# Optimization experiments

Measured on AMD Instinct MI355X. Metric: run time of the kernel, lower is better.

Reference implementation:

```python
import jax, jax.numpy as jnp
import numpy as np

B, NPG, C = 16, 4096, 256          # graphs, nodes per graph per type, feat dim
N = B * NPG                        # nodes per type
E = N * 16                         # edges per edge type (avg degree 16)
RATIO = 0.25
K = int(np.ceil(RATIO * NPG))      # top-k nodes per graph per type


def setup_inputs() -> dict:
    key = jax.random.key(0)
    ks = jax.random.split(key, 16)
    s = 1.0 / np.sqrt(C)
    inp = {
        "x_inst": jax.random.normal(ks[0], (N, C), jnp.float32),
        "x_data": jax.random.normal(ks[1], (N, C), jnp.float32),
        "w_kqv_inst": jax.random.normal(ks[2], (C, 3), jnp.float32) * s,
        "b_kqv_inst": jnp.zeros((3,), jnp.float32),
        "w_kqv_data": jax.random.normal(ks[3], (C, 3), jnp.float32) * s,
        "b_kqv_data": jnp.zeros((3,), jnp.float32),
        "w_out_inst": jax.random.normal(ks[4], (1, 1), jnp.float32),
        "b_out_inst": jnp.zeros((1,), jnp.float32),
        "w_out_data": jax.random.normal(ks[5], (1, 1), jnp.float32),
        "b_out_data": jnp.zeros((1,), jnp.float32),
        "krel_w": jax.random.normal(ks[6], (3,), jnp.float32),
        "krel_b": jnp.zeros((3,), jnp.float32),
        "vrel_w": jax.random.normal(ks[7], (3,), jnp.float32),
        "vrel_b": jnp.zeros((3,), jnp.float32),
        "p_rel": jnp.ones((3,), jnp.float32),
        "ei_i2d": jax.random.randint(ks[8], (2, E), 0, N, jnp.int32),
        "ei_d2i": jax.random.randint(ks[9], (2, E), 0, N, jnp.int32),
        "ei_i2i": jax.random.randint(ks[10], (2, E), 0, N, jnp.int32),
        "batch_inst": jnp.repeat(jnp.arange(B, dtype=jnp.int32), NPG),
        "batch_data": jnp.repeat(jnp.arange(B, dtype=jnp.int32), NPG),
    }
    return inp


def _hgt_scores(x_inst, x_data, w_kqv_inst, b_kqv_inst, w_kqv_data, b_kqv_data,
                w_out_inst, b_out_inst, w_out_data, b_out_data,
                krel_w, krel_b, vrel_w, vrel_b, p_rel,
                ei_i2d, ei_d2i, ei_i2i):
    # HGTConv with out_channels=1, heads=1 -> H=1, D=1 (k,q,v scalar per node)
    kqv_i = x_inst @ w_kqv_inst + b_kqv_inst   # [N,3]
    kqv_d = x_data @ w_kqv_data + b_kqv_data
    k_i, q_i, v_i = kqv_i[:, 0], kqv_i[:, 1], kqv_i[:, 2]
    k_d, q_d, v_d = kqv_d[:, 0], kqv_d[:, 1], kqv_d[:, 2]
    # dst offsets follow node-type order: inst=0, data=N
    q_glob = jnp.concatenate([q_i, q_d])       # [2N]
    Ntot = 2 * N

    def edge_terms(k_src, v_src, ei, t, dst_off):
        s, d = ei[0], ei[1]
        ke = k_src[s] * krel_w[t] + krel_b[t]  # per-relation 1x1 k_rel
        ve = v_src[s] * vrel_w[t] + vrel_b[t]  # per-relation 1x1 v_rel
        dg = d + dst_off
        logit = q_glob[dg] * ke * p_rel[t]     # (q_i*k_j).sum * p_rel / sqrt(D=1)
        return logit, ve, dg

    l0, v0, d0 = edge_terms(k_i, v_i, ei_i2d, 0, N)  # inst->data (dst=data)
    l1, v1, d1 = edge_terms(k_d, v_d, ei_d2i, 1, 0)  # data->inst (dst=inst)
    l2, v2, d2 = edge_terms(k_i, v_i, ei_i2i, 2, 0)  # inst->inst (dst=inst)
    logits = jnp.concatenate([l0, l1, l2])
    vals = jnp.concatenate([v0, v1, v2])
    dst = jnp.concatenate([d0, d1, d2])

    # segment softmax over incoming edges of each destination node
    m = jax.ops.segment_max(logits, dst, num_segments=Ntot)
    m = jnp.where(jnp.isfinite(m), m, 0.0)
    ex = jnp.exp(logits - m[dst])
    den = jax.ops.segment_sum(ex, dst, num_segments=Ntot)
    alpha = ex / den[dst]
    a = jax.ops.segment_sum(alpha * vals, dst, num_segments=Ntot)  # [2N]

    # out_lin (1->1) per node type; skip inactive (1 != 256); GELU (exact)
    s_i = jax.nn.gelu(a[:N, None] * w_out_inst[0, 0] + b_out_inst, approximate=False)
    s_d = jax.nn.gelu(a[N:, None] * w_out_data[0, 0] + b_out_data, approximate=False)
    return s_i, s_d  # [N,1] each


def _pool(x, score):
    # per-graph top-k on score, gate by tanh(score), mean over selected
    sv = score[:, 0].reshape(B, NPG)
    xv = x.reshape(B, NPG, -1)
    topv, topi = jax.lax.top_k(sv, K)                      # [B,K]
    xs = jnp.take_along_axis(xv, topi[:, :, None], axis=1)  # [B,K,C]
    return (xs * jnp.tanh(topv)[:, :, None]).mean(axis=1)   # [B,C]


def reference(x_inst, x_data, w_kqv_inst, b_kqv_inst, w_kqv_data, b_kqv_data,
              w_out_inst, b_out_inst, w_out_data, b_out_data,
              krel_w, krel_b, vrel_w, vrel_b, p_rel,
              ei_i2d, ei_d2i, ei_i2i, batch_inst, batch_data):
    # batch_* are uniform [B x NPG] blocks; pooling uses reshape equivalently.
    s_i, s_d = _hgt_scores(x_inst, x_data, w_kqv_inst, b_kqv_inst,
                           w_kqv_data, b_kqv_data, w_out_inst, b_out_inst,
                           w_out_data, b_out_data, krel_w, krel_b,
                           vrel_w, vrel_b, p_rel, ei_i2d, ei_d2i, ei_i2i)
    return jnp.concatenate([_pool(x_inst, s_i), _pool(x_data, s_d)], axis=-1)  # [B, 2C]
```

## Files before the change

### kernel.cpp

```cpp
#include <hip/hip_runtime.h>
#include <math.h>

constexpr int BB   = 16;
constexpr int NPGc = 4096;
constexpr int Cc   = 256;
constexpr int Nc   = BB * NPGc;
constexpr int Ec   = Nc * 16;
constexpr int Kc   = 1024;
constexpr int NBUK = 512;
constexpr int BUKW = 256;
constexpr int CHUNK = 8192;
constexpr int NCHUNK = (3 * Ec) / CHUNK;

__device__ __forceinline__ unsigned fkey(float f) {
    int b = __float_as_int(f);
    unsigned u = (unsigned)b;
    return (b < 0) ? ~u : (u | 0x80000000u);
}
__device__ __forceinline__ float inv_fkey(unsigned u) {
    unsigned b = (u & 0x80000000u) ? (u ^ 0x80000000u) : ~u;
    return __int_as_float((int)b);
}

__global__ __launch_bounds__(256) void kqv_kernel(
    const float* __restrict__ x_inst, const float* __restrict__ x_data,
    const float* __restrict__ w_inst, const float* __restrict__ b_inst,
    const float* __restrict__ w_data, const float* __restrict__ b_data,
    float2* __restrict__ kv_i, float2* __restrict__ kv_d,
    float* __restrict__ q_glob)
{
    int tid  = threadIdx.x;
    int wave = tid >> 6, lane = tid & 63;
    int grp  = lane >> 4, l = lane & 15;
    int g    = blockIdx.x * 16 + wave * 4 + grp;
    int row0 = g * 2;
    int side = (row0 >= Nc) ? 1 : 0;
    int node0 = row0 - side * Nc;
    const float* x  = side ? x_data : x_inst;
    const float* w  = side ? w_data : w_inst;
    const float* bp = side ? b_data : b_inst;
    float2* kv = side ? kv_d : kv_i;

    float wr[48];
#pragma unroll
    for (int it = 0; it < 4; ++it) {
        const float4* wv = (const float4*)(w + (it * 64 + l * 4) * 3);
        float4 f0 = wv[0], f1 = wv[1], f2 = wv[2];
        wr[it*12+0]=f0.x; wr[it*12+1]=f0.y; wr[it*12+2]=f0.z; wr[it*12+3]=f0.w;
        wr[it*12+4]=f1.x; wr[it*12+5]=f1.y; wr[it*12+6]=f1.z; wr[it*12+7]=f1.w;
        wr[it*12+8]=f2.x; wr[it*12+9]=f2.y; wr[it*12+10]=f2.z; wr[it*12+11]=f2.w;
    }
    float b0 = bp[0], b1 = bp[1], b2 = bp[2];

    const float4* rp = (const float4*)(x + (size_t)node0 * Cc);
    float4 xv[2][4];
#pragma unroll
    for (int r = 0; r < 2; ++r)
#pragma unroll
        for (int it = 0; it < 4; ++it)
            xv[r][it] = rp[r * 64 + it * 16 + l];

#pragma unroll
    for (int r = 0; r < 2; ++r) {
        float kk = 0.f, qq = 0.f, vv = 0.f;
#pragma unroll
        for (int it = 0; it < 4; ++it) {
            float xs[4] = {xv[r][it].x, xv[r][it].y, xv[r][it].z, xv[r][it].w};
#pragma unroll
            for (int u = 0; u < 4; ++u) {
                float xd = xs[u];
                kk = fmaf(xd, wr[it * 12 + u * 3 + 0], kk);
                qq = fmaf(xd, wr[it * 12 + u * 3 + 1], qq);
                vv = fmaf(xd, wr[it * 12 + u * 3 + 2], vv);
            }
        }
#pragma unroll
        for (int off = 8; off; off >>= 1) {
            kk += __shfl_xor(kk, off, 64);
            qq += __shfl_xor(qq, off, 64);
            vv += __shfl_xor(vv, off, 64);
        }
        if (l == 0) {
            int node = node0 + r;
            kv[node] = make_float2(kk + b0, vv + b2);
            q_glob[side * Nc + node] = qq + b1;
        }
    }
}

__global__ __launch_bounds__(256) void count_kernel(
    const int* __restrict__ ei0, const int* __restrict__ ei1,
    const int* __restrict__ ei2, unsigned* __restrict__ bucket_cnt)
{
    __shared__ unsigned hist[NBUK];
    int tid = threadIdx.x;
    for (int j = tid; j < NBUK; j += 256) hist[j] = 0;
    __syncthreads();
    unsigned base = blockIdx.x * (unsigned)CHUNK;
    int t = (int)(base >> 20);
    unsigned i0 = base & (unsigned)(Ec - 1);
    const int* ei = (t == 0) ? ei0 : (t == 1) ? ei1 : ei2;
    int off = (t == 0) ? Nc : 0;
    const int4* dv = (const int4*)(ei + Ec + i0);
#pragma unroll 4
    for (int j = 0; j < CHUNK / 1024; ++j) {
        int4 d4 = dv[j * 256 + tid];
        atomicAdd(&hist[(unsigned)(d4.x + off) >> 8], 1u);
        atomicAdd(&hist[(unsigned)(d4.y + off) >> 8], 1u);
        atomicAdd(&hist[(unsigned)(d4.z + off) >> 8], 1u);
        atomicAdd(&hist[(unsigned)(d4.w + off) >> 8], 1u);
    }
    __syncthreads();
    for (int j = tid; j < NBUK; j += 256)
        if (hist[j]) atomicAdd(&bucket_cnt[j], hist[j]);
}

__global__ __launch_bounds__(NBUK) void scan_kernel(
    const unsigned* __restrict__ bucket_cnt,
    unsigned* __restrict__ bucket_base, unsigned* __restrict__ bucket_fill)
{
    __shared__ unsigned s[NBUK];
    int t = threadIdx.x;
    unsigned mine = bucket_cnt[t];
    s[t] = mine;
    __syncthreads();
    for (int off = 1; off < NBUK; off <<= 1) {
        unsigned v = (t >= off) ? s[t - off] : 0u;
        __syncthreads();
        s[t] += v;
        __syncthreads();
    }
    unsigned ex = s[t] - mine;
    bucket_base[t] = ex;
    bucket_fill[t] = ex;
    if (t == NBUK - 1) bucket_base[NBUK] = s[t];
}

__global__ __launch_bounds__(256) void fill_kernel(
    const int* __restrict__ ei0, const int* __restrict__ ei1,
    const int* __restrict__ ei2, unsigned* __restrict__ bucket_fill,
    unsigned* __restrict__ sorted)
{
    __shared__ unsigned hist[NBUK];
    __shared__ unsigned res[NBUK];
    int tid = threadIdx.x;
    for (int j = tid; j < NBUK; j += 256) hist[j] = 0;
    __syncthreads();
    unsigned base = blockIdx.x * (unsigned)CHUNK;
    int t = (int)(base >> 20);
    unsigned i0 = base & (unsigned)(Ec - 1);
    const int* ei = (t == 0) ? ei0 : (t == 1) ? ei1 : ei2;
    int off = (t == 0) ? Nc : 0;
    const int4* dv = (const int4*)(ei + Ec + i0);
    const int4* sv = (const int4*)(ei + i0);
#pragma unroll 4
    for (int j = 0; j < CHUNK / 1024; ++j) {
        int4 d4 = dv[j * 256 + tid];
        atomicAdd(&hist[(unsigned)(d4.x + off) >> 8], 1u);
        atomicAdd(&hist[(unsigned)(d4.y + off) >> 8], 1u);
        atomicAdd(&hist[(unsigned)(d4.z + off) >> 8], 1u);
        atomicAdd(&hist[(unsigned)(d4.w + off) >> 8], 1u);
    }
    __syncthreads();
    for (int j = tid; j < NBUK; j += 256) {
        unsigned h = hist[j];
        res[j] = h ? atomicAdd(&bucket_fill[j], h) : 0u;
    }
    __syncthreads();
#pragma unroll 4
    for (int j = 0; j < CHUNK / 1024; ++j) {
        int4 d4 = dv[j * 256 + tid];
        int4 s4 = sv[j * 256 + tid];
        int dd[4] = {d4.x, d4.y, d4.z, d4.w};
        int ss[4] = {s4.x, s4.y, s4.z, s4.w};
#pragma unroll
        for (int u = 0; u < 4; ++u) {
            int dg  = dd[u] + off;
            int bkt = dg >> 8;
            unsigned pos = atomicAdd(&res[bkt], 1u);
            sorted[pos] =
                (unsigned)ss[u] | ((unsigned)t << 16) | ((unsigned)(dg & 255) << 18);
        }
    }
}

__global__ __launch_bounds__(512) void bucket_accum_kernel(
    const unsigned* __restrict__ bucket_base, const unsigned* __restrict__ sorted,
    const float* __restrict__ krel_w, const float* __restrict__ krel_b,
    const float* __restrict__ vrel_w, const float* __restrict__ vrel_b,
    const float* __restrict__ p_rel,
    const float2* __restrict__ kv_i, const float2* __restrict__ kv_d,
    const float* __restrict__ q_glob,
    float* __restrict__ den, float* __restrict__ num)
{
    __shared__ float den_l[2 * BUKW];
    __shared__ float num_l[2 * BUKW];
    __shared__ float q_l[BUKW];
    int tid = threadIdx.x;
    int b   = blockIdx.x;
    den_l[tid] = 0.0f; num_l[tid] = 0.0f;
    if (tid < BUKW) q_l[tid] = q_glob[b * BUKW + tid];
    float kw0 = krel_w[0], kw1 = krel_w[1], kw2 = krel_w[2];
    float kb0 = krel_b[0], kb1 = krel_b[1], kb2 = krel_b[2];
    float vw0 = vrel_w[0], vw1 = vrel_w[1], vw2 = vrel_w[2];
    float vb0 = vrel_b[0], vb1 = vrel_b[1], vb2 = vrel_b[2];
    float pr0 = p_rel[0],  pr1 = p_rel[1],  pr2 = p_rel[2];
    unsigned beg = bucket_base[b], end = bucket_base[b + 1];
    int rep = tid & 1;
    __syncthreads();

    for (unsigned e = beg + tid; e < end; e += 512) {
        unsigned r = sorted[e];
        int s    = (int)(r & 0xFFFFu);
        int t    = (int)((r >> 16) & 3u);
        int low8 = (int)((r >> 18) & 255u);
        float2 kvv = (t == 1) ? kv_d[s] : kv_i[s];
        float kwt = (t == 0) ? kw0 : (t == 1) ? kw1 : kw2;
        float kbt = (t == 0) ? kb0 : (t == 1) ? kb1 : kb2;
        float vwt = (t == 0) ? vw0 : (t == 1) ? vw1 : vw2;
        float vbt = (t == 0) ? vb0 : (t == 1) ? vb1 : vb2;
        float prt = (t == 0) ? pr0 : (t == 1) ? pr1 : pr2;
        float ke = fmaf(kvv.x, kwt, kbt);
        float ve = fmaf(kvv.y, vwt, vbt);
        float logit = q_l[low8] * ke * prt;
        float ex = __expf(fminf(logit, 80.0f));
        int slot = low8 * 2 + rep;
        __hip_atomic_fetch_add(&den_l[slot], ex, __ATOMIC_RELAXED,
                               __HIP_MEMORY_SCOPE_WORKGROUP);
        __hip_atomic_fetch_add(&num_l[slot], ex * ve, __ATOMIC_RELAXED,
                               __HIP_MEMORY_SCOPE_WORKGROUP);
    }
    __syncthreads();
    if (tid < BUKW) {
        den[b * BUKW + tid] = den_l[tid * 2] + den_l[tid * 2 + 1];
        num[b * BUKW + tid] = num_l[tid * 2] + num_l[tid * 2 + 1];
    }
}

__global__ __launch_bounds__(1024) void select_kernel(
    const float* __restrict__ den, const float* __restrict__ num,
    const float* __restrict__ w_out_inst, const float* __restrict__ b_out_inst,
    const float* __restrict__ w_out_data, const float* __restrict__ b_out_data,
    int* __restrict__ sel_idx, float* __restrict__ sel_w)
{
    __shared__ unsigned keys[NPGc];
    __shared__ unsigned hist[2048];
    __shared__ unsigned wsum[16];
    __shared__ unsigned short cand[NPGc];
    __shared__ unsigned sh_bin1, sh_rem1, sh_bin2, sh_rem2, sh_cnt, sh_nc;

    int tid  = threadIdx.x;
    int seg  = blockIdx.x;
    int side = seg >> 4;
    int b    = seg & 15;
    float wo = side ? w_out_data[0] : w_out_inst[0];
    float bo = side ? b_out_data[0] : b_out_inst[0];
    int base_node = side * Nc + b * NPGc;
    int base_sel  = seg * Kc;

    unsigned myk[4]; int myj[4];
#pragma unroll
    for (int p = 0; p < 4; ++p) {
        int j = p * 1024 + tid;
        float dn = den[base_node + j];
        float a  = (dn > 0.0f) ? num[base_node + j] / dn : 0.0f;
        float z  = fmaf(a, wo, bo);
        float s  = 0.5f * z * (1.0f + erff(z * 0.70710678f));
        unsigned k32 = fkey(s);
        keys[j] = k32; myk[p] = k32; myj[p] = j;
    }
    if (tid == 0) { sh_cnt = 0; sh_nc = 0; }
    hist[tid] = 0; hist[tid + 1024] = 0;
    __syncthreads();

#pragma unroll
    for (int p = 0; p < 4; ++p) atomicAdd(&hist[myk[p] >> 21], 1u);
    __syncthreads();
    {
        unsigned g0 = hist[2047 - 2 * tid];
        unsigned g1 = hist[2046 - 2 * tid];
        unsigned x = g0 + g1;
        int lane = tid & 63;
#pragma unroll
        for (int off = 1; off < 64; off <<= 1) {
            unsigned y = __shfl_up(x, off, 64);
            if (lane >= off) x += y;
        }
        if (lane == 63) wsum[tid >> 6] = x;
        __syncthreads();
        if (tid < 16) {
            unsigned v = wsum[tid];
#pragma unroll
            for (int off = 1; off < 16; off <<= 1) {
                unsigned y = __shfl_up(v, off, 64);
                if (tid >= off) v += y;
            }
            wsum[tid] = v;
        }
        __syncthreads();
        unsigned basew = (tid >= 64) ? wsum[(tid >> 6) - 1] : 0u;
        unsigned incl  = basew + x;
        unsigned incl0 = incl - g1;
        unsigned K = Kc;
        if (incl0 >= K && incl0 - g0 < K) { sh_bin1 = 2047 - 2 * tid; sh_rem1 = K - (incl0 - g0); }
        if (incl  >= K && incl0     < K) { sh_bin1 = 2046 - 2 * tid; sh_rem1 = K - incl0; }
    }
    __syncthreads();
    unsigned bin1 = sh_bin1, rem1 = sh_rem1;
    hist[tid] = 0; hist[tid + 1024] = 0;
    __syncthreads();

#pragma unroll
    for (int p = 0; p < 4; ++p)
        if ((myk[p] >> 21) == bin1)
            atomicAdd(&hist[(myk[p] >> 10) & 2047u], 1u);
    __syncthreads();
    {
        unsigned g0 = hist[2047 - 2 * tid];
        unsigned g1 = hist[2046 - 2 * tid];
        unsigned x = g0 + g1;
        int lane = tid & 63;
#pragma unroll
        for (int off = 1; off < 64; off <<= 1) {
            unsigned y = __shfl_up(x, off, 64);
            if (lane >= off) x += y;
        }
        if (lane == 63) wsum[tid >> 6] = x;
        __syncthreads();
        if (tid < 16) {
            unsigned v = wsum[tid];
#pragma unroll
            for (int off = 1; off < 16; off <<= 1) {
                unsigned y = __shfl_up(v, off, 64);
                if (tid >= off) v += y;
            }
            wsum[tid] = v;
        }
        __syncthreads();
        unsigned basew = (tid >= 64) ? wsum[(tid >> 6) - 1] : 0u;
        unsigned incl  = basew + x;
        unsigned incl0 = incl - g1;
        unsigned K = rem1;
        if (incl0 >= K && incl0 - g0 < K) { sh_bin2 = 2047 - 2 * tid; sh_rem2 = K - (incl0 - g0); }
        if (incl  >= K && incl0     < K) { sh_bin2 = 2046 - 2 * tid; sh_rem2 = K - incl0; }
    }
    __syncthreads();
    unsigned pref22 = (bin1 << 11) | sh_bin2;
    unsigned rem2 = sh_rem2;

#pragma unroll
    for (int p = 0; p < 4; ++p) {
        unsigned top22 = myk[p] >> 10;
        if (top22 > pref22) {
            unsigned pos = atomicAdd(&sh_cnt, 1u);
            sel_idx[base_sel + pos] = myj[p];
            sel_w[base_sel + pos]   = tanhf(inv_fkey(myk[p]));
        } else if (top22 == pref22) {
            unsigned cp = atomicAdd(&sh_nc, 1u);
            cand[cp] = (unsigned short)myj[p];
        }
    }
    __syncthreads();

    unsigned nc = sh_nc;
    for (unsigned c = tid; c < nc; c += 1024) {
        int j = cand[c];
        unsigned k32 = keys[j];
        unsigned rank = 0;
        for (unsigned q = 0; q < nc; ++q) {
            int jq = cand[q];
            unsigned kq = keys[jq];
            rank += (kq > k32 || (kq == k32 && jq < j)) ? 1u : 0u;
        }
        if (rank < rem2) {
            unsigned pos = atomicAdd(&sh_cnt, 1u);
            sel_idx[base_sel + pos] = j;
            sel_w[base_sel + pos]   = tanhf(inv_fkey(k32));
        }
    }
}

__global__ __launch_bounds__(1024) void pool_kernel(
    const float* __restrict__ x_inst, const float* __restrict__ x_data,
    const int* __restrict__ sel_idx, const float* __restrict__ sel_w,
    float* __restrict__ out)
{
    __shared__ int   ridx[64];
    __shared__ float rw[64];
    __shared__ float accs[256];
    int tid   = threadIdx.x;
    int blk   = blockIdx.x;
    int seg   = blk >> 4;
    int chunk = blk & 15;
    int side  = seg >> 4;
    int b     = seg & 15;
    if (tid < 64) {
        ridx[tid] = sel_idx[seg * Kc + chunk * 64 + tid];
        rw[tid]   = sel_w[seg * Kc + chunk * 64 + tid];
    }
    if (tid < 256) accs[tid] = 0.0f;
    __syncthreads();
    const float* x = side ? x_data : x_inst;
    int w = tid >> 6, l = tid & 63;
    float ax = 0.f, ay = 0.f, az = 0.f, aw = 0.f;
#pragma unroll
    for (int r = 0; r < 4; ++r) {
        int   row = ridx[w * 4 + r];
        float wt  = rw[w * 4 + r];
        float4 xv = ((const float4*)(x + ((size_t)(b * NPGc + row)) * Cc))[l];
        ax = fmaf(xv.x, wt, ax); ay = fmaf(xv.y, wt, ay);
        az = fmaf(xv.z, wt, az); aw = fmaf(xv.w, wt, aw);
    }
    atomicAdd(&accs[l * 4 + 0], ax);
    atomicAdd(&accs[l * 4 + 1], ay);
    atomicAdd(&accs[l * 4 + 2], az);
    atomicAdd(&accs[l * 4 + 3], aw);
    __syncthreads();
    if (tid < 256)
        unsafeAtomicAdd(&out[b * 512 + side * 256 + tid], accs[tid] * (1.0f / (float)Kc));
}

extern "C" void kernel_launch(void* const* d_in, const int* in_sizes, int n_in,
                              void* d_out, int out_size, void* d_ws, size_t ws_size,
                              hipStream_t stream) {
    const float* x_inst     = (const float*)d_in[0];
    const float* x_data     = (const float*)d_in[1];
    const float* w_kqv_inst = (const float*)d_in[2];
    const float* b_kqv_inst = (const float*)d_in[3];
    const float* w_kqv_data = (const float*)d_in[4];
    const float* b_kqv_data = (const float*)d_in[5];
    const float* w_out_inst = (const float*)d_in[6];
    const float* b_out_inst = (const float*)d_in[7];
    const float* w_out_data = (const float*)d_in[8];
    const float* b_out_data = (const float*)d_in[9];
    const float* krel_w     = (const float*)d_in[10];
    const float* krel_b     = (const float*)d_in[11];
    const float* vrel_w     = (const float*)d_in[12];
    const float* vrel_b     = (const float*)d_in[13];
    const float* p_rel      = (const float*)d_in[14];
    const int*   ei_i2d     = (const int*)d_in[15];
    const int*   ei_d2i     = (const int*)d_in[16];
    const int*   ei_i2i     = (const int*)d_in[17];
    float* out = (float*)d_out;

    char* ws = (char*)d_ws;
    float2* kv_i   = (float2*)ws;
    float2* kv_d   = kv_i + Nc;
    float*  q_glob = (float*)(kv_d + Nc);
    float*  den    = q_glob + 2 * Nc;
    float*  num    = den + 2 * Nc;
    unsigned* bucket_cnt  = (unsigned*)(num + 2 * Nc);
    unsigned* bucket_base = bucket_cnt + NBUK;
    unsigned* bucket_fill = bucket_base + NBUK + 1;
    int*      sel_idx     = (int*)(bucket_fill + NBUK);
    float*    sel_w       = (float*)(sel_idx + 32 * Kc);
    unsigned* sorted      = (unsigned*)(sel_w + 32 * Kc);

    hipMemsetAsync(bucket_cnt, 0, NBUK * sizeof(unsigned), stream);
    hipMemsetAsync(d_out, 0, (size_t)out_size * sizeof(float), stream);

    count_kernel<<<NCHUNK, 256, 0, stream>>>(ei_i2d, ei_d2i, ei_i2i, bucket_cnt);
    scan_kernel<<<1, NBUK, 0, stream>>>(bucket_cnt, bucket_base, bucket_fill);
    fill_kernel<<<NCHUNK, 256, 0, stream>>>(ei_i2d, ei_d2i, ei_i2i,
                                            bucket_fill, sorted);

    kqv_kernel<<<(2 * Nc) / 32, 256, 0, stream>>>(
        x_inst, x_data, w_kqv_inst, b_kqv_inst, w_kqv_data, b_kqv_data,
        kv_i, kv_d, q_glob);

    bucket_accum_kernel<<<NBUK, 512, 0, stream>>>(
        bucket_base, sorted,
        krel_w, krel_b, vrel_w, vrel_b, p_rel,
        kv_i, kv_d, q_glob, den, num);

    select_kernel<<<32, 1024, 0, stream>>>(
        den, num, w_out_inst, b_out_inst, w_out_data, b_out_data,
        sel_idx, sel_w);

    pool_kernel<<<512, 1024, 0, stream>>>(x_inst, x_data, sel_idx, sel_w, out);
}
```

Baseline: 306.7 us.

## Rework kqv weight staging, cache fill dst indices, widen accumulation blocks

The kqv kernel now stages the weight matrix in shared memory and has each 16-lane group compute four rows instead of two, so each weight load is reused across more rows and the launch uses half as many blocks. The fill kernel keeps destination indices in registers between the histogram and scatter passes instead of reading them from global memory twice. Edge chunks are halved, giving twice as many count and fill blocks. The bucket accumulation kernel moves to 1024 threads with four LDS replica slots per node to spread atomic contention. The trade-offs are more register pressure and different occupancy, plus more global atomics on the bucket counters.

```diff
diff --git a/kernel.cpp b/kernel.cpp
--- a/kernel.cpp
+++ b/kernel.cpp
@@ -9,7 +9,7 @@
 constexpr int Kc   = 1024;
 constexpr int NBUK = 512;
 constexpr int BUKW = 256;
-constexpr int CHUNK = 8192;
+constexpr int CHUNK = 4096;
 constexpr int NCHUNK = (3 * Ec) / CHUNK;
 
 __device__ __forceinline__ unsigned fkey(float f) {
@@ -29,11 +29,12 @@
     float2* __restrict__ kv_i, float2* __restrict__ kv_d,
     float* __restrict__ q_glob)
 {
+    __shared__ float wls[768];
     int tid  = threadIdx.x;
     int wave = tid >> 6, lane = tid & 63;
     int grp  = lane >> 4, l = lane & 15;
     int g    = blockIdx.x * 16 + wave * 4 + grp;
-    int row0 = g * 2;
+    int row0 = g * 4;
     int side = (row0 >= Nc) ? 1 : 0;
     int node0 = row0 - side * Nc;
     const float* x  = side ? x_data : x_inst;
@@ -41,49 +42,59 @@
     const float* bp = side ? b_data : b_inst;
     float2* kv = side ? kv_d : kv_i;
 
-    float wr[48];
-#pragma unroll
-    for (int it = 0; it < 4; ++it) {
-        const float4* wv = (const float4*)(w + (it * 64 + l * 4) * 3);
-        float4 f0 = wv[0], f1 = wv[1], f2 = wv[2];
-        wr[it*12+0]=f0.x; wr[it*12+1]=f0.y; wr[it*12+2]=f0.z; wr[it*12+3]=f0.w;
-        wr[it*12+4]=f1.x; wr[it*12+5]=f1.y; wr[it*12+6]=f1.z; wr[it*12+7]=f1.w;
-        wr[it*12+8]=f2.x; wr[it*12+9]=f2.y; wr[it*12+10]=f2.z; wr[it*12+11]=f2.w;
-    }
+    if (tid < 192)
+        ((float4*)wls)[tid] = ((const float4*)w)[tid];
     float b0 = bp[0], b1 = bp[1], b2 = bp[2];
+    __syncthreads();
 
     const float4* rp = (const float4*)(x + (size_t)node0 * Cc);
-    float4 xv[2][4];
-#pragma unroll
-    for (int r = 0; r < 2; ++r)
+    float4 xv[4][4];
+#pragma unroll
+    for (int r = 0; r < 4; ++r)
 #pragma unroll
         for (int it = 0; it < 4; ++it)
             xv[r][it] = rp[r * 64 + it * 16 + l];
 
-#pragma unroll
-    for (int r = 0; r < 2; ++r) {
-        float kk = 0.f, qq = 0.f, vv = 0.f;
-#pragma unroll
-        for (int it = 0; it < 4; ++it) {
-            float xs[4] = {xv[r][it].x, xv[r][it].y, xv[r][it].z, xv[r][it].w};
-#pragma unroll
-            for (int u = 0; u < 4; ++u) {
-                float xd = xs[u];
-                kk = fmaf(xd, wr[it * 12 + u * 3 + 0], kk);
-                qq = fmaf(xd, wr[it * 12 + u * 3 + 1], qq);
-                vv = fmaf(xd, wr[it * 12 + u * 3 + 2], vv);
-            }
-        }
+    float kk[4] = {0.f, 0.f, 0.f, 0.f};
+    float qq[4] = {0.f, 0.f, 0.f, 0.f};
+    float vv[4] = {0.f, 0.f, 0.f, 0.f};
+    const float4* wv4 = (const float4*)wls;
+#pragma unroll
+    for (int it = 0; it < 4; ++it) {
+        float4 w0 = wv4[it * 48 + l * 3 + 0];
+        float4 w1 = wv4[it * 48 + l * 3 + 1];
+        float4 w2 = wv4[it * 48 + l * 3 + 2];
+#pragma unroll
+        for (int r = 0; r < 4; ++r) {
+            float x0 = xv[r][it].x, x1 = xv[r][it].y;
+            float x2 = xv[r][it].z, x3 = xv[r][it].w;
+            kk[r] = fmaf(x0, w0.x, kk[r]);
+            qq[r] = fmaf(x0, w0.y, qq[r]);
+            vv[r] = fmaf(x0, w0.z, vv[r]);
+            kk[r] = fmaf(x1, w0.w, kk[r]);
+            qq[r] = fmaf(x1, w1.x, qq[r]);
+            vv[r] = fmaf(x1, w1.y, vv[r]);
+            kk[r] = fmaf(x2, w1.z, kk[r]);
+            qq[r] = fmaf(x2, w1.w, qq[r]);
+            vv[r] = fmaf(x2, w2.x, vv[r]);
+            kk[r] = fmaf(x3, w2.y, kk[r]);
+            qq[r] = fmaf(x3, w2.z, qq[r]);
+            vv[r] = fmaf(x3, w2.w, vv[r]);
+        }
+    }
+
+#pragma unroll
+    for (int r = 0; r < 4; ++r) {
 #pragma unroll
         for (int off = 8; off; off >>= 1) {
-            kk += __shfl_xor(kk, off, 64);
-            qq += __shfl_xor(qq, off, 64);
-            vv += __shfl_xor(vv, off, 64);
+            kk[r] += __shfl_xor(kk[r], off, 64);
+            qq[r] += __shfl_xor(qq[r], off, 64);
+            vv[r] += __shfl_xor(vv[r], off, 64);
         }
         if (l == 0) {
             int node = node0 + r;
-            kv[node] = make_float2(kk + b0, vv + b2);
-            q_glob[side * Nc + node] = qq + b1;
+            kv[node] = make_float2(kk[r] + b0, vv[r] + b2);
+            q_glob[side * Nc + node] = qq[r] + b1;
         }
     }
 }
@@ -102,7 +113,7 @@
     const int* ei = (t == 0) ? ei0 : (t == 1) ? ei1 : ei2;
     int off = (t == 0) ? Nc : 0;
     const int4* dv = (const int4*)(ei + Ec + i0);
-#pragma unroll 4
+#pragma unroll
     for (int j = 0; j < CHUNK / 1024; ++j) {
         int4 d4 = dv[j * 256 + tid];
         atomicAdd(&hist[(unsigned)(d4.x + off) >> 8], 1u);
@@ -153,9 +164,11 @@
     int off = (t == 0) ? Nc : 0;
     const int4* dv = (const int4*)(ei + Ec + i0);
     const int4* sv = (const int4*)(ei + i0);
-#pragma unroll 4
+    int4 dreg[CHUNK / 1024];
+#pragma unroll
     for (int j = 0; j < CHUNK / 1024; ++j) {
         int4 d4 = dv[j * 256 + tid];
+        dreg[j] = d4;
         atomicAdd(&hist[(unsigned)(d4.x + off) >> 8], 1u);
         atomicAdd(&hist[(unsigned)(d4.y + off) >> 8], 1u);
         atomicAdd(&hist[(unsigned)(d4.z + off) >> 8], 1u);
@@ -167,9 +180,9 @@
         res[j] = h ? atomicAdd(&bucket_fill[j], h) : 0u;
     }
     __syncthreads();
-#pragma unroll 4
+#pragma unroll
     for (int j = 0; j < CHUNK / 1024; ++j) {
-        int4 d4 = dv[j * 256 + tid];
+        int4 d4 = dreg[j];
         int4 s4 = sv[j * 256 + tid];
         int dd[4] = {d4.x, d4.y, d4.z, d4.w};
         int ss[4] = {s4.x, s4.y, s4.z, s4.w};
@@ -184,7 +197,7 @@
     }
 }
 
-__global__ __launch_bounds__(512) void bucket_accum_kernel(
+__global__ __launch_bounds__(1024) void bucket_accum_kernel(
     const unsigned* __restrict__ bucket_base, const unsigned* __restrict__ sorted,
     const float* __restrict__ krel_w, const float* __restrict__ krel_b,
     const float* __restrict__ vrel_w, const float* __restrict__ vrel_b,
@@ -193,8 +206,8 @@
     const float* __restrict__ q_glob,
     float* __restrict__ den, float* __restrict__ num)
 {
-    __shared__ float den_l[2 * BUKW];
-    __shared__ float num_l[2 * BUKW];
+    __shared__ float den_l[4 * BUKW];
+    __shared__ float num_l[4 * BUKW];
     __shared__ float q_l[BUKW];
     int tid = threadIdx.x;
     int b   = blockIdx.x;
@@ -206,10 +219,10 @@
     float vb0 = vrel_b[0], vb1 = vrel_b[1], vb2 = vrel_b[2];
     float pr0 = p_rel[0],  pr1 = p_rel[1],  pr2 = p_rel[2];
     unsigned beg = bucket_base[b], end = bucket_base[b + 1];
-    int rep = tid & 1;
-    __syncthreads();
-
-    for (unsigned e = beg + tid; e < end; e += 512) {
+    int rep = tid & 3;
+    __syncthreads();
+
+    for (unsigned e = beg + tid; e < end; e += 1024) {
         unsigned r = sorted[e];
         int s    = (int)(r & 0xFFFFu);
         int t    = (int)((r >> 16) & 3u);
@@ -224,7 +237,7 @@
         float ve = fmaf(kvv.y, vwt, vbt);
         float logit = q_l[low8] * ke * prt;
         float ex = __expf(fminf(logit, 80.0f));
-        int slot = low8 * 2 + rep;
+        int slot = low8 * 4 + rep;
         __hip_atomic_fetch_add(&den_l[slot], ex, __ATOMIC_RELAXED,
                                __HIP_MEMORY_SCOPE_WORKGROUP);
         __hip_atomic_fetch_add(&num_l[slot], ex * ve, __ATOMIC_RELAXED,
@@ -232,8 +245,10 @@
     }
     __syncthreads();
     if (tid < BUKW) {
-        den[b * BUKW + tid] = den_l[tid * 2] + den_l[tid * 2 + 1];
-        num[b * BUKW + tid] = num_l[tid * 2] + num_l[tid * 2 + 1];
+        den[b * BUKW + tid] = (den_l[tid * 4] + den_l[tid * 4 + 1]) +
+                              (den_l[tid * 4 + 2] + den_l[tid * 4 + 3]);
+        num[b * BUKW + tid] = (num_l[tid * 4] + num_l[tid * 4 + 1]) +
+                              (num_l[tid * 4 + 2] + num_l[tid * 4 + 3]);
     }
 }
 
@@ -464,11 +479,11 @@
     fill_kernel<<<NCHUNK, 256, 0, stream>>>(ei_i2d, ei_d2i, ei_i2i,
                                             bucket_fill, sorted);
 
-    kqv_kernel<<<(2 * Nc) / 32, 256, 0, stream>>>(
+    kqv_kernel<<<(2 * Nc) / 64, 256, 0, stream>>>(
         x_inst, x_data, w_kqv_inst, b_kqv_inst, w_kqv_data, b_kqv_data,
         kv_i, kv_d, q_glob);
 
-    bucket_accum_kernel<<<NBUK, 512, 0, stream>>>(
+    bucket_accum_kernel<<<NBUK, 1024, 0, stream>>>(
         bucket_base, sorted,
         krel_w, krel_b, vrel_w, vrel_b, p_rel,
         kv_i, kv_d, q_glob, den, num);
```

Result: slower. 316.9 us (+3.3%).
